# Kernel tuning notes

Hardware: AMD Instinct MI355X
Metric: run time of the kernel (lower is better)

## Reference

```python
import jax, jax.numpy as jnp
import numpy as np

N, IN_DIM, EMB = 65536, 768, 128
CB_SIZES = [8, 64, 512]
COMMIT = 0.25  # standard EMA-VQ commitment cost


def setup_inputs() -> dict:
    key = jax.random.key(0)
    ks = jax.random.split(key, 12)
    s = 0.02
    return {
        "x": jax.random.normal(ks[0], (N, IN_DIM), jnp.float32),
        "W_e1": jax.random.normal(ks[1], (IN_DIM, IN_DIM), jnp.float32) * s,
        "b_e1": jnp.zeros((IN_DIM,), jnp.float32),
        "W_e2": jax.random.normal(ks[2], (EMB, IN_DIM), jnp.float32) * s,
        "b_e2": jnp.zeros((EMB,), jnp.float32),
        "W_d1": jax.random.normal(ks[3], (EMB, EMB), jnp.float32) * s,
        "b_d1": jnp.zeros((EMB,), jnp.float32),
        "W_d2": jax.random.normal(ks[4], (EMB, EMB), jnp.float32) * s,
        "b_d2": jnp.zeros((EMB,), jnp.float32),
        "E0": jax.random.normal(ks[5], (CB_SIZES[0], EMB), jnp.float32),
        "E1": jax.random.normal(ks[6], (CB_SIZES[1], EMB), jnp.float32),
        "E2": jax.random.normal(ks[7], (CB_SIZES[2], EMB), jnp.float32),
    }


def _quantize(r, E):
    # squared L2 distances [N, K] = |r|^2 - 2 r.E^T + |E|^2
    d = (jnp.sum(r * r, axis=-1, keepdims=True)
         - 2.0 * jnp.einsum("nd,kd->nk", r, E)
         + jnp.sum(E * E, axis=-1))
    idx = jnp.argmin(d, axis=-1)          # [N]
    z_q = E[idx]                           # gather [N, EMB]
    loss = COMMIT * jnp.mean((jax.lax.stop_gradient(z_q) - r) ** 2)
    z_q_st = r + jax.lax.stop_gradient(z_q - r)  # straight-through
    return z_q_st, loss, idx


def reference(x, W_e1, b_e1, W_e2, b_e2, W_d1, b_d1, W_d2, b_d2, E0, E1, E2):
    # encoder MLP
    h = jax.nn.relu(x @ W_e1.T + b_e1)
    z = h @ W_e2.T + b_e2                 # [N, EMB]

    residual = z
    quantized_sum = jnp.zeros_like(z)
    total_loss = jnp.float32(0.0)
    all_indices = []
    for E in (E0, E1, E2):                # fixed depth=3 residual VQ loop
        z_q, loss, idx = _quantize(residual, E)
        residual = residual - z_q
        quantized_sum = quantized_sum + z_q
        total_loss = total_loss + loss
        all_indices.append(idx)

    # decoder MLP
    h2 = jax.nn.relu(quantized_sum @ W_d1.T + b_d1)
    reconstructed = h2 @ W_d2.T + b_d2    # [N, EMB]
    codes = jnp.stack(all_indices, axis=1)  # [N, depth]
    return reconstructed, total_loss, codes
```

## Files before the change

### kernel.cpp

```cpp
#include <hip/hip_runtime.h>

typedef _Float16 f16;
typedef __attribute__((ext_vector_type(4))) _Float16 f16x4;
typedef __attribute__((ext_vector_type(8))) _Float16 f16x8;
typedef __attribute__((ext_vector_type(4))) float    f32x4;

static constexpr int NROWS = 65536;
static constexpr int D_IN  = 768;
static constexpr int D_EMB = 128;
static constexpr long LOSS_OFF  = (long)NROWS * D_EMB;
static constexpr long CODES_OFF = LOSS_OFF + 1;

static constexpr long WOFF = 201326592L;
static constexpr long WE1H = 0,       WE1L = 589824;
static constexpr long WE2H = 1179648, WE2L = 1277952;
static constexpr long WD1F = 1376256, WD2F = 1392640;
static constexpr long E0H = 1409024, E0L = 1410048;
static constexpr long E1H = 1411072, E1L = 1419264;
static constexpr long E2H = 1427456, E2L = 1492992;
static constexpr long PARTIAL_B = WOFF + 4194304L;
static constexpr long NORM_B    = WOFF + 4198400L;

__device__ __forceinline__ float dot4(float4 a, float4 b){
  return fmaf(a.x,b.x, fmaf(a.y,b.y, fmaf(a.z,b.z, a.w*b.w)));
}

__device__ __forceinline__ void split4(float4 v, f16x4& hi, f16x4& lo){
  _Float16 h0=(_Float16)v.x, h1=(_Float16)v.y, h2=(_Float16)v.z, h3=(_Float16)v.w;
  hi[0]=h0; hi[1]=h1; hi[2]=h2; hi[3]=h3;
  lo[0]=(_Float16)((v.x-(float)h0)*2048.0f);
  lo[1]=(_Float16)((v.y-(float)h1)*2048.0f);
  lo[2]=(_Float16)((v.z-(float)h2)*2048.0f);
  lo[3]=(_Float16)((v.w-(float)h3)*2048.0f);
}

__device__ __forceinline__ void split8_reg(const float* v, f16x8& hi, f16x8& lo){
#pragma unroll
  for (int i = 0; i < 8; i++){
    _Float16 h = (_Float16)v[i];
    hi[i] = h;
    lo[i] = (_Float16)((v[i]-(float)h)*2048.0f);
  }
}

__global__ __launch_bounds__(256)
void split_weights_kernel(const float* __restrict__ We1, const float* __restrict__ We2,
                          const float* __restrict__ Wd1, const float* __restrict__ Wd2,
                          const float* __restrict__ E0,  const float* __restrict__ E1,
                          const float* __restrict__ E2,  f16* __restrict__ wp){
  int t = blockIdx.x*256 + threadIdx.x;
  if (t >= 198912) return;
  const float* src; long o4; long hO, lO; bool dual = true;
  if      (t < 147456){ src=We1; o4=t;        hO=WE1H; lO=WE1L; }
  else if (t < 172032){ src=We2; o4=t-147456; hO=WE2H; lO=WE2L; }
  else if (t < 176128){ src=Wd1; o4=t-172032; hO=WD1F; lO=0; dual=false; }
  else if (t < 180224){ src=Wd2; o4=t-176128; hO=WD2F; lO=0; dual=false; }
  else if (t < 180480){ src=E0;  o4=t-180224; hO=E0H;  lO=E0L; }
  else if (t < 182528){ src=E1;  o4=t-180480; hO=E1H;  lO=E1L; }
  else                { src=E2;  o4=t-182528; hO=E2H;  lO=E2L; }
  float4 v = *(const float4*)(src + o4*4);
  if (dual){
    f16x4 h4, l4; split4(v, h4, l4);
    *(f16x4*)(wp + hO + o4*4) = h4;
    *(f16x4*)(wp + lO + o4*4) = l4;
  } else {
    f16x4 h4; h4[0]=(_Float16)v.x; h4[1]=(_Float16)v.y; h4[2]=(_Float16)v.z; h4[3]=(_Float16)v.w;
    *(f16x4*)(wp + hO + o4*4) = h4;
  }
}

__global__ __launch_bounds__(256)
void enorm_kernel(const float* __restrict__ E0, const float* __restrict__ E1,
                  const float* __restrict__ E2, float* __restrict__ norms){
  int t = blockIdx.x*256 + threadIdx.x;
  if (t >= 584) return;
  const float* row;
  if (t < 8)       row = E0 + (long)t*128;
  else if (t < 72) row = E1 + (long)(t-8)*128;
  else             row = E2 + (long)(t-72)*128;
  float q[4];
#pragma unroll
  for (int sq = 0; sq < 4; sq++){
    float s = 0.f;
#pragma unroll
    for (int j = 0; j < 8; j++){
      float4 v = *(const float4*)(row + sq*32 + j*4);
      s += dot4(v, v);
    }
    q[sq] = s;
  }
  norms[t] = ((q[0] + q[1]) + q[2]) + q[3];
}

template<bool RELU>
__global__ __launch_bounds__(512, 2)
void gemm_v2_kernel(const float* __restrict__ A,
                    const f16* __restrict__ Bhg, const f16* __restrict__ Blg,
                    const float* __restrict__ bias, float* __restrict__ C,
                    int M, int N, int K){
  constexpr int RS = 40;
  __shared__ f16 AhL[2][256*RS];
  __shared__ f16 AlL[2][256*RS];
  __shared__ f16 BhL[2][128*RS];
  __shared__ f16 BlL[2][128*RS];

  const int tid = threadIdx.x;
  const int wave = tid >> 6, lane = tid & 63;
  const int wm = wave >> 1, wn = wave & 1;
  const int lr = lane & 15, lg = lane >> 4;

  const int gx  = gridDim.x;
  const int lid = blockIdx.y * gx + blockIdx.x;
  const int xcd = lid & 7;
  const int rr  = lid >> 3;
  const int bx  = rr % gx;
  const int by  = (rr / gx) * 8 + xcd;

  const long m0 = (long)by * 256;
  const long n0 = (long)bx * 128;

  const int ar = tid >> 3;
  const int ac = tid & 7;
  const int br = tid >> 2;
  const int bkc = tid & 3;

  const int nt = K >> 5;

  float4 pa[4];
  f16x8 pbh, pbl;

#pragma unroll
  for (int i = 0; i < 4; i++)
    pa[i] = *(const float4*)(A + (m0 + i*64 + ar)*K + ac*4);
  pbh = *(const f16x8*)(Bhg + (n0 + br)*K + bkc*8);
  pbl = *(const f16x8*)(Blg + (n0 + br)*K + bkc*8);

#pragma unroll
  for (int i = 0; i < 4; i++){
    f16x4 h4, l4; split4(pa[i], h4, l4);
    *(f16x4*)&AhL[0][(i*64 + ar)*RS + ac*4] = h4;
    *(f16x4*)&AlL[0][(i*64 + ar)*RS + ac*4] = l4;
  }
  *(f16x8*)&BhL[0][br*RS + bkc*8] = pbh;
  *(f16x8*)&BlL[0][br*RS + bkc*8] = pbl;
  __syncthreads();

  f32x4 accm[4][4], accc[4][4];
#pragma unroll
  for (int i = 0; i < 4; i++)
#pragma unroll
    for (int j = 0; j < 4; j++){
      accm[i][j] = (f32x4){0.f,0.f,0.f,0.f};
      accc[i][j] = (f32x4){0.f,0.f,0.f,0.f};
    }

  int cur = 0;
  for (int t = 0; t < nt; t++){
    const bool more = (t + 1 < nt);
    if (more){
      const long ko = (long)(t+1) * 32;
#pragma unroll
      for (int i = 0; i < 4; i++)
        pa[i] = *(const float4*)(A + (m0 + i*64 + ar)*K + ko + ac*4);
      pbh = *(const f16x8*)(Bhg + (n0 + br)*K + ko + bkc*8);
      pbl = *(const f16x8*)(Blg + (n0 + br)*K + ko + bkc*8);
    }

    f16x8 ah[4], al[4];
#pragma unroll
    for (int mi = 0; mi < 4; mi++){
      int row = wm*64 + mi*16 + lr;
      ah[mi] = *(const f16x8*)&AhL[cur][row*RS + lg*8];
      al[mi] = *(const f16x8*)&AlL[cur][row*RS + lg*8];
    }
#pragma unroll
    for (int ni = 0; ni < 4; ni++){
      int col = wn*64 + ni*16 + lr;
      f16x8 bh = *(const f16x8*)&BhL[cur][col*RS + lg*8];
      f16x8 bl = *(const f16x8*)&BlL[cur][col*RS + lg*8];
#pragma unroll
      for (int mi = 0; mi < 4; mi++){
        accm[mi][ni] = __builtin_amdgcn_mfma_f32_16x16x32_f16(ah[mi], bh, accm[mi][ni], 0, 0, 0);
        accc[mi][ni] = __builtin_amdgcn_mfma_f32_16x16x32_f16(ah[mi], bl, accc[mi][ni], 0, 0, 0);
        accc[mi][ni] = __builtin_amdgcn_mfma_f32_16x16x32_f16(al[mi], bh, accc[mi][ni], 0, 0, 0);
      }
    }

    if (more){
      int nb = cur ^ 1;
#pragma unroll
      for (int i = 0; i < 4; i++){
        f16x4 h4, l4; split4(pa[i], h4, l4);
        *(f16x4*)&AhL[nb][(i*64 + ar)*RS + ac*4] = h4;
        *(f16x4*)&AlL[nb][(i*64 + ar)*RS + ac*4] = l4;
      }
      *(f16x8*)&BhL[nb][br*RS + bkc*8] = pbh;
      *(f16x8*)&BlL[nb][br*RS + bkc*8] = pbl;
      __syncthreads();
      cur = nb;
    }
  }

  float bv[4];
#pragma unroll
  for (int ni = 0; ni < 4; ni++) bv[ni] = bias[n0 + wn*64 + ni*16 + lr];
#pragma unroll
  for (int mi = 0; mi < 4; mi++){
#pragma unroll
    for (int ni = 0; ni < 4; ni++){
#pragma unroll
      for (int r = 0; r < 4; r++){
        float v = accm[mi][ni][r] + accc[mi][ni][r]*(1.0f/2048.0f) + bv[ni];
        if (RELU) v = fmaxf(v, 0.f);
        long row = m0 + wm*64 + mi*16 + lg*4 + r;
        C[row*N + n0 + wn*64 + ni*16 + lr] = v;
      }
    }
  }
}

template<bool RELU, bool OUT16>
__global__ __launch_bounds__(256)
void gemm_f16_dec(const f16* __restrict__ Ag, const f16* __restrict__ Bg,
                  const float* __restrict__ bias,
                  float* __restrict__ C32, f16* __restrict__ C16, int M){
  constexpr int RS = 136;
  __shared__ f16 As[128*RS];
  __shared__ f16 Bs[128*RS];
  const int tid = threadIdx.x;
  const int wave = tid >> 6, lane = tid & 63;
  const int wm = wave >> 1, wn = wave & 1;
  const int lr = lane & 15, lg = lane >> 4;
  const long m0 = (long)blockIdx.y * 128;
  const int srow = tid >> 1, sco = (tid & 1) * 64;

#pragma unroll
  for (int c = 0; c < 8; c++){
    *(f16x8*)&As[srow*RS + sco + c*8] = *(const f16x8*)(Ag + (m0+srow)*128 + sco + c*8);
    *(f16x8*)&Bs[srow*RS + sco + c*8] = *(const f16x8*)(Bg + (long)srow*128 + sco + c*8);
  }
  __syncthreads();

  f32x4 acc[4][4];
#pragma unroll
  for (int i = 0; i < 4; i++)
#pragma unroll
    for (int j = 0; j < 4; j++) acc[i][j] = (f32x4){0.f,0.f,0.f,0.f};

#pragma unroll
  for (int ks = 0; ks < 4; ks++){
    f16x8 a[4];
#pragma unroll
    for (int mi = 0; mi < 4; mi++)
      a[mi] = *(const f16x8*)&As[(wm*64 + mi*16 + lr)*RS + ks*32 + lg*8];
#pragma unroll
    for (int ni = 0; ni < 4; ni++){
      f16x8 b = *(const f16x8*)&Bs[(wn*64 + ni*16 + lr)*RS + ks*32 + lg*8];
#pragma unroll
      for (int mi = 0; mi < 4; mi++)
        acc[mi][ni] = __builtin_amdgcn_mfma_f32_16x16x32_f16(a[mi], b, acc[mi][ni], 0, 0, 0);
    }
  }

  float bv[4];
#pragma unroll
  for (int ni = 0; ni < 4; ni++) bv[ni] = bias[wn*64 + ni*16 + lr];
#pragma unroll
  for (int mi = 0; mi < 4; mi++){
#pragma unroll
    for (int ni = 0; ni < 4; ni++){
#pragma unroll
      for (int r = 0; r < 4; r++){
        float v = acc[mi][ni][r] + bv[ni];
        if (RELU) v = fmaxf(v, 0.f);
        long row = m0 + wm*64 + mi*16 + lg*4 + r;
        long col = wn*64 + ni*16 + lr;
        if (OUT16) C16[row*128 + col] = (_Float16)v;
        else       C32[row*128 + col] = v;
      }
    }
  }
}

__global__ __launch_bounds__(256)
void vq_mfma_kernel(const float* __restrict__ z,
                    const float* __restrict__ E0c, const float* __restrict__ E1c,
                    const float* __restrict__ E2c,
                    const f16* __restrict__ wp, const float* __restrict__ normg,
                    f16* __restrict__ q16, float* __restrict__ out,
                    float* __restrict__ partial){
  constexpr int VS = 132;
  constexpr int ES = 136;
  __shared__ float rs[64*VS];
  __shared__ f16 Eh[64*ES];
  __shared__ f16 El[64*ES];
  __shared__ float pE[64];
  __shared__ int   besti[3*64];
  __shared__ float wsum[4];

  const int tid  = threadIdx.x;
  const int wave = tid >> 6, lane = tid & 63;
  const int lr = lane & 15, lg = lane >> 4;
  const int row0 = blockIdx.x * 64;
  const int urow = tid & 63, uq = tid >> 6;
  const int sc = tid & 63, sq = tid >> 6;

#pragma unroll
  for (int i = 0; i < 8; i++){
    int idx = i*256 + tid;
    int r = idx >> 5, c = (idx & 31) * 4;
    *(float4*)&rs[r*VS + c] = *(const float4*)&z[(long)(row0 + r)*D_EMB + c];
  }

  float4 qa[8];
#pragma unroll
  for (int j = 0; j < 8; j++) qa[j] = make_float4(0.f,0.f,0.f,0.f);
  float lsum = 0.f;

  const float* Etab[3] = {E0c, E1c, E2c};
  const int    Ktab[3] = {8, 64, 512};
  const long   EHt[3]  = {E0H, E1H, E2H};
  const long   ELt[3]  = {E0L, E1L, E2L};
  const int    NOt[3]  = {0, 8, 72};

  for (int l = 0; l < 3; l++){
    const float* E = Etab[l];
    const int K = Ktab[l];
    const f16* Ehg = wp + EHt[l];
    const f16* Elg = wp + ELt[l];
    const float* nrm = normg + NOt[l];

    __syncthreads();
    f16x8 ah[4], al[4];
#pragma unroll
    for (int ks = 0; ks < 4; ks++){
      float av[8];
      *(float4*)&av[0] = *(const float4*)&rs[(wave*16 + lr)*VS + ks*32 + lg*8];
      *(float4*)&av[4] = *(const float4*)&rs[(wave*16 + lr)*VS + ks*32 + lg*8 + 4];
      split8_reg(av, ah[ks], al[ks]);
    }

    float bd[4]; int bi[4];
#pragma unroll
    for (int r = 0; r < 4; r++){ bd[r] = 3.0e38f; bi[r] = 0x7fffffff; }

    for (int kbase = 0; kbase < K; kbase += 64){
      const int cn = (K - kbase < 64) ? (K - kbase) : 64;
      __syncthreads();
      if (sc < cn){
        long go = (long)(kbase + sc)*D_EMB + sq*32;
#pragma unroll
        for (int j = 0; j < 4; j++){
          *(f16x8*)&Eh[sc*ES + sq*32 + j*8] = *(const f16x8*)(Ehg + go + j*8);
          *(f16x8*)&El[sc*ES + sq*32 + j*8] = *(const f16x8*)(Elg + go + j*8);
        }
        if (sq == 0) pE[sc] = nrm[kbase + sc];
      } else {
        f16x8 zz;
#pragma unroll
        for (int i = 0; i < 8; i++) zz[i] = (_Float16)0.f;
#pragma unroll
        for (int j = 0; j < 4; j++){
          *(f16x8*)&Eh[sc*ES + sq*32 + j*8] = zz;
          *(f16x8*)&El[sc*ES + sq*32 + j*8] = zz;
        }
        if (sq == 0) pE[sc] = 3.0e38f;
      }
      __syncthreads();

      const int cgmax = (cn + 15) >> 4;
      for (int cg = 0; cg < cgmax; cg++){
        f32x4 Sm = (f32x4){0.f,0.f,0.f,0.f};
        f32x4 Sc = (f32x4){0.f,0.f,0.f,0.f};
#pragma unroll
        for (int ks = 0; ks < 4; ks++){
          f16x8 bh = *(const f16x8*)&Eh[(cg*16 + lr)*ES + ks*32 + lg*8];
          f16x8 bl = *(const f16x8*)&El[(cg*16 + lr)*ES + ks*32 + lg*8];
          Sm = __builtin_amdgcn_mfma_f32_16x16x32_f16(ah[ks], bh, Sm, 0, 0, 0);
          Sc = __builtin_amdgcn_mfma_f32_16x16x32_f16(ah[ks], bl, Sc, 0, 0, 0);
          Sc = __builtin_amdgcn_mfma_f32_16x16x32_f16(al[ks], bh, Sc, 0, 0, 0);
        }
        int code = cg*16 + lr;
        float ne = pE[code];
        int kg = kbase + code;
#pragma unroll
        for (int r = 0; r < 4; r++){
          float S  = fmaf(Sc[r], 1.0f/2048.0f, Sm[r]);
          float sd = fmaf(-2.0f, S, ne);
          if (sd < bd[r]){ bd[r] = sd; bi[r] = kg; }
        }
      }
    }

#pragma unroll
    for (int r = 0; r < 4; r++){
#pragma unroll
      for (int off = 1; off < 16; off <<= 1){
        float ob = __shfl_xor(bd[r], off, 16);
        int   oi = __shfl_xor(bi[r], off, 16);
        if (ob < bd[r] || (ob == bd[r] && oi < bi[r])){ bd[r] = ob; bi[r] = oi; }
      }
      if (lr == 0) besti[l*64 + wave*16 + lg*4 + r] = bi[r];
    }
    __syncthreads();

    {
      int k = besti[l*64 + urow];
      const float* Er = E + (long)k*D_EMB + uq*32;
#pragma unroll
      for (int j = 0; j < 8; j++){
        float4 e = *(const float4*)&Er[j*4];
        float* rp = &rs[urow*VS + uq*32 + j*4];
        float4 r = *(const float4*)rp;
        float4 df = make_float4(e.x-r.x, e.y-r.y, e.z-r.z, e.w-r.w);
        lsum += dot4(df, df);
        *(float4*)rp = make_float4(r.x-e.x, r.y-e.y, r.z-e.z, r.w-e.w);
        qa[j].x += e.x; qa[j].y += e.y; qa[j].z += e.z; qa[j].w += e.w;
      }
    }
  }

  __syncthreads();
#pragma unroll
  for (int j = 0; j < 8; j++)
    *(float4*)&rs[urow*VS + uq*32 + j*4] = qa[j];
  __syncthreads();
#pragma unroll
  for (int i = 0; i < 8; i++){
    int idx = i*256 + tid;
    int r = idx >> 5, c = (idx & 31) * 4;
    float4 v = *(const float4*)&rs[r*VS + c];
    f16x4 h4; h4[0]=(_Float16)v.x; h4[1]=(_Float16)v.y; h4[2]=(_Float16)v.z; h4[3]=(_Float16)v.w;
    *(f16x4*)&q16[(long)(row0 + r)*D_EMB + c] = h4;
  }
  if (tid < 64){
    long n = row0 + tid;
    for (int l = 0; l < 3; l++)
      out[CODES_OFF + n*3 + l] = (float)besti[l*64 + tid];
  }
  for (int off = 32; off > 0; off >>= 1) lsum += __shfl_down(lsum, off);
  if ((tid & 63) == 0) wsum[tid >> 6] = lsum;
  __syncthreads();
  if (tid == 0) partial[blockIdx.x] = wsum[0] + wsum[1] + wsum[2] + wsum[3];
}

__global__ __launch_bounds__(256)
void loss_reduce_kernel(const float* __restrict__ partial, float* __restrict__ out){
  __shared__ float ws2[4];
  int tid = threadIdx.x;
  float s = 0.f;
  for (int i = tid; i < 1024; i += 256) s += partial[i];
  for (int off = 32; off > 0; off >>= 1) s += __shfl_down(s, off);
  if ((tid & 63) == 0) ws2[tid >> 6] = s;
  __syncthreads();
  if (tid == 0)
    out[LOSS_OFF] = (ws2[0] + ws2[1] + ws2[2] + ws2[3]) * (0.25f / (float)((long)NROWS * D_EMB));
}

extern "C" void kernel_launch(void* const* d_in, const int* in_sizes, int n_in,
                              void* d_out, int out_size, void* d_ws, size_t ws_size,
                              hipStream_t stream) {
  (void)in_sizes; (void)n_in; (void)out_size; (void)ws_size;
  const float* x   = (const float*)d_in[0];
  const float* We1 = (const float*)d_in[1];
  const float* be1 = (const float*)d_in[2];
  const float* We2 = (const float*)d_in[3];
  const float* be2 = (const float*)d_in[4];
  const float* Wd1 = (const float*)d_in[5];
  const float* bd1 = (const float*)d_in[6];
  const float* Wd2 = (const float*)d_in[7];
  const float* bd2 = (const float*)d_in[8];
  const float* E0  = (const float*)d_in[9];
  const float* E1  = (const float*)d_in[10];
  const float* E2  = (const float*)d_in[11];
  float* out = (float*)d_out;
  char*  ws  = (char*)d_ws;

  float* h    = (float*)ws;
  f16*   q16  = (f16*)ws;
  f16*   h216 = (f16*)(ws + 33554432L);
  f16*   wp   = (f16*)(ws + WOFF);
  float* partial = (float*)(ws + PARTIAL_B);
  float* norms   = (float*)(ws + NORM_B);
  float* z = out;

  dim3 blk(256);
  split_weights_kernel<<<dim3(777), blk, 0, stream>>>(We1, We2, Wd1, Wd2, E0, E1, E2, wp);
  enorm_kernel<<<dim3(3), blk, 0, stream>>>(E0, E1, E2, norms);
  gemm_v2_kernel<true ><<<dim3(D_IN/128,  NROWS/256), dim3(512), 0, stream>>>(
      x, wp+WE1H, wp+WE1L, be1, h, NROWS, D_IN,  D_IN);
  gemm_v2_kernel<false><<<dim3(D_EMB/128, NROWS/256), dim3(512), 0, stream>>>(
      h, wp+WE2H, wp+WE2L, be2, z, NROWS, D_EMB, D_IN);
  vq_mfma_kernel<<<dim3(NROWS/64), blk, 0, stream>>>(z, E0, E1, E2, wp, norms, q16, out, partial);
  loss_reduce_kernel<<<dim3(1), blk, 0, stream>>>(partial, out);
  gemm_f16_dec<true, true ><<<dim3(1, NROWS/128), blk, 0, stream>>>(q16,  wp+WD1F, bd1, nullptr, h216, NROWS);
  gemm_f16_dec<false,false><<<dim3(1, NROWS/128), blk, 0, stream>>>(h216, wp+WD2F, bd2, out, nullptr, NROWS);
}
```

Before: 454.1 us.

## Fuse encoder second GEMM, residual VQ and decoder MLP into one kernel

Replaces the separate z-GEMM, VQ and two decoder GEMM launches with one kernel per 128-row tile. The kernel computes z with a split-fp16 MFMA GEMM over h, runs the three-level quantization on the LDS-resident residual, then applies both decoder layers from shared memory. This removes the global round trips of z, q16 and h2 and three kernel launches. The cost is a large LDS arena (about 134 KB), which limits occupancy to one block per CU. The z GEMM now runs on only 512 blocks, each covering all 128 output columns.

```diff
diff --git a/kernel.cpp b/kernel.cpp
--- a/kernel.cpp
+++ b/kernel.cpp
@@ -219,103 +219,152 @@
   }
 }
 
-template<bool RELU, bool OUT16>
 __global__ __launch_bounds__(256)
-void gemm_f16_dec(const f16* __restrict__ Ag, const f16* __restrict__ Bg,
-                  const float* __restrict__ bias,
-                  float* __restrict__ C32, f16* __restrict__ C16, int M){
-  constexpr int RS = 136;
-  __shared__ f16 As[128*RS];
-  __shared__ f16 Bs[128*RS];
-  const int tid = threadIdx.x;
+void fused_zvqdec_kernel(const float* __restrict__ hg,
+                         const f16* __restrict__ Bhg, const f16* __restrict__ Blg,
+                         const float* __restrict__ be2,
+                         const float* __restrict__ E0c, const float* __restrict__ E1c,
+                         const float* __restrict__ E2c,
+                         const f16* __restrict__ wp, const float* __restrict__ normg,
+                         const float* __restrict__ bd1g, const float* __restrict__ bd2g,
+                         float* __restrict__ out, float* __restrict__ partial){
+  __shared__ __align__(16) char arena[137280];
+  constexpr int VS = 132;
+  constexpr int ES = 136;
+
+  const int tid  = threadIdx.x;
   const int wave = tid >> 6, lane = tid & 63;
   const int wm = wave >> 1, wn = wave & 1;
   const int lr = lane & 15, lg = lane >> 4;
-  const long m0 = (long)blockIdx.y * 128;
-  const int srow = tid >> 1, sco = (tid & 1) * 64;
-
-#pragma unroll
-  for (int c = 0; c < 8; c++){
-    *(f16x8*)&As[srow*RS + sco + c*8] = *(const f16x8*)(Ag + (m0+srow)*128 + sco + c*8);
-    *(f16x8*)&Bs[srow*RS + sco + c*8] = *(const f16x8*)(Bg + (long)srow*128 + sco + c*8);
-  }
-  __syncthreads();
-
-  f32x4 acc[4][4];
-#pragma unroll
-  for (int i = 0; i < 4; i++)
-#pragma unroll
-    for (int j = 0; j < 4; j++) acc[i][j] = (f32x4){0.f,0.f,0.f,0.f};
-
-#pragma unroll
-  for (int ks = 0; ks < 4; ks++){
-    f16x8 a[4];
+  const long row0 = (long)blockIdx.x * 128;
+
+  float* rs = (float*)arena;
+  f16*  Eh  = (f16*)(arena + 67584);
+  f16*  El  = (f16*)(arena + 84992);
+  float* pE = (float*)(arena + 102400);
+  int*  besti = (int*)(arena + 102656);
+  float* wsum = (float*)(arena + 104192);
+  f16*  W1  = (f16*)(arena + 67584);
+  f16*  W2  = (f16*)(arena + 102400);
+  f16*  h2p = (f16*)arena;
+
+  {
+    constexpr int RS = 40;
+    f16* base = (f16*)arena;
+    f16* AhL = base;
+    f16* AlL = base + 10240;
+    f16* BhL = base + 20480;
+    f16* BlL = base + 30720;
+    const int K = D_IN;
+    const int srow = tid >> 3, sc4 = tid & 7;
+    const int prow = tid >> 1, pkc = (tid & 1)*2;
+
+    float4 pa[4];
+    f16x8 pbh[2], pbl[2];
+#pragma unroll
+    for (int p = 0; p < 4; p++)
+      pa[p] = *(const float4*)(hg + (row0 + p*32 + srow)*K + sc4*4);
+#pragma unroll
+    for (int c = 0; c < 2; c++){
+      pbh[c] = *(const f16x8*)(Bhg + (long)prow*K + (pkc+c)*8);
+      pbl[c] = *(const f16x8*)(Blg + (long)prow*K + (pkc+c)*8);
+    }
+#pragma unroll
+    for (int p = 0; p < 4; p++){
+      f16x4 h4, l4; split4(pa[p], h4, l4);
+      *(f16x4*)&AhL[(p*32 + srow)*RS + sc4*4] = h4;
+      *(f16x4*)&AlL[(p*32 + srow)*RS + sc4*4] = l4;
+    }
+#pragma unroll
+    for (int c = 0; c < 2; c++){
+      *(f16x8*)&BhL[prow*RS + (pkc+c)*8] = pbh[c];
+      *(f16x8*)&BlL[prow*RS + (pkc+c)*8] = pbl[c];
+    }
+    __syncthreads();
+
+    f32x4 accm[4][4], accc[4][4];
+#pragma unroll
+    for (int i = 0; i < 4; i++)
+#pragma unroll
+      for (int j = 0; j < 4; j++){
+        accm[i][j] = (f32x4){0.f,0.f,0.f,0.f};
+        accc[i][j] = (f32x4){0.f,0.f,0.f,0.f};
+      }
+
+    const int nt = K >> 5;
+    int cur = 0;
+    for (int t = 0; t < nt; t++){
+      const bool more = (t + 1 < nt);
+      if (more){
+        const long ko = (long)(t+1)*32;
+#pragma unroll
+        for (int p = 0; p < 4; p++)
+          pa[p] = *(const float4*)(hg + (row0 + p*32 + srow)*K + ko + sc4*4);
+#pragma unroll
+        for (int c = 0; c < 2; c++){
+          pbh[c] = *(const f16x8*)(Bhg + (long)prow*K + ko + (pkc+c)*8);
+          pbl[c] = *(const f16x8*)(Blg + (long)prow*K + ko + (pkc+c)*8);
+        }
+      }
+      f16x8 ah[4], al[4];
+#pragma unroll
+      for (int mi = 0; mi < 4; mi++){
+        int row = wm*64 + mi*16 + lr;
+        ah[mi] = *(const f16x8*)&AhL[cur*5120 + row*RS + lg*8];
+        al[mi] = *(const f16x8*)&AlL[cur*5120 + row*RS + lg*8];
+      }
+#pragma unroll
+      for (int ni = 0; ni < 4; ni++){
+        int col = wn*64 + ni*16 + lr;
+        f16x8 bh = *(const f16x8*)&BhL[cur*5120 + col*RS + lg*8];
+        f16x8 bl = *(const f16x8*)&BlL[cur*5120 + col*RS + lg*8];
+#pragma unroll
+        for (int mi = 0; mi < 4; mi++){
+          accm[mi][ni] = __builtin_amdgcn_mfma_f32_16x16x32_f16(ah[mi], bh, accm[mi][ni], 0, 0, 0);
+          accc[mi][ni] = __builtin_amdgcn_mfma_f32_16x16x32_f16(ah[mi], bl, accc[mi][ni], 0, 0, 0);
+          accc[mi][ni] = __builtin_amdgcn_mfma_f32_16x16x32_f16(al[mi], bh, accc[mi][ni], 0, 0, 0);
+        }
+      }
+      if (more){
+        int nb = cur ^ 1;
+#pragma unroll
+        for (int p = 0; p < 4; p++){
+          f16x4 h4, l4; split4(pa[p], h4, l4);
+          *(f16x4*)&AhL[nb*5120 + (p*32 + srow)*RS + sc4*4] = h4;
+          *(f16x4*)&AlL[nb*5120 + (p*32 + srow)*RS + sc4*4] = l4;
+        }
+#pragma unroll
+        for (int c = 0; c < 2; c++){
+          *(f16x8*)&BhL[nb*5120 + prow*RS + (pkc+c)*8] = pbh[c];
+          *(f16x8*)&BlL[nb*5120 + prow*RS + (pkc+c)*8] = pbl[c];
+        }
+        __syncthreads();
+        cur = nb;
+      }
+    }
+
+    __syncthreads();
+    float bv[4];
+#pragma unroll
+    for (int ni = 0; ni < 4; ni++) bv[ni] = be2[wn*64 + ni*16 + lr];
 #pragma unroll
     for (int mi = 0; mi < 4; mi++)
-      a[mi] = *(const f16x8*)&As[(wm*64 + mi*16 + lr)*RS + ks*32 + lg*8];
-#pragma unroll
-    for (int ni = 0; ni < 4; ni++){
-      f16x8 b = *(const f16x8*)&Bs[(wn*64 + ni*16 + lr)*RS + ks*32 + lg*8];
-#pragma unroll
-      for (int mi = 0; mi < 4; mi++)
-        acc[mi][ni] = __builtin_amdgcn_mfma_f32_16x16x32_f16(a[mi], b, acc[mi][ni], 0, 0, 0);
-    }
-  }
-
-  float bv[4];
-#pragma unroll
-  for (int ni = 0; ni < 4; ni++) bv[ni] = bias[wn*64 + ni*16 + lr];
-#pragma unroll
-  for (int mi = 0; mi < 4; mi++){
-#pragma unroll
-    for (int ni = 0; ni < 4; ni++){
-#pragma unroll
-      for (int r = 0; r < 4; r++){
-        float v = acc[mi][ni][r] + bv[ni];
-        if (RELU) v = fmaxf(v, 0.f);
-        long row = m0 + wm*64 + mi*16 + lg*4 + r;
-        long col = wn*64 + ni*16 + lr;
-        if (OUT16) C16[row*128 + col] = (_Float16)v;
-        else       C32[row*128 + col] = v;
-      }
-    }
-  }
-}
-
-__global__ __launch_bounds__(256)
-void vq_mfma_kernel(const float* __restrict__ z,
-                    const float* __restrict__ E0c, const float* __restrict__ E1c,
-                    const float* __restrict__ E2c,
-                    const f16* __restrict__ wp, const float* __restrict__ normg,
-                    f16* __restrict__ q16, float* __restrict__ out,
-                    float* __restrict__ partial){
-  constexpr int VS = 132;
-  constexpr int ES = 136;
-  __shared__ float rs[64*VS];
-  __shared__ f16 Eh[64*ES];
-  __shared__ f16 El[64*ES];
-  __shared__ float pE[64];
-  __shared__ int   besti[3*64];
-  __shared__ float wsum[4];
-
-  const int tid  = threadIdx.x;
-  const int wave = tid >> 6, lane = tid & 63;
-  const int lr = lane & 15, lg = lane >> 4;
-  const int row0 = blockIdx.x * 64;
-  const int urow = tid & 63, uq = tid >> 6;
+#pragma unroll
+      for (int ni = 0; ni < 4; ni++)
+#pragma unroll
+        for (int r = 0; r < 4; r++){
+          float v = accm[mi][ni][r] + accc[mi][ni][r]*(1.0f/2048.0f) + bv[ni];
+          rs[(wm*64 + mi*16 + lg*4 + r)*VS + wn*64 + ni*16 + lr] = v;
+        }
+  }
+
+  float4 qa[16];
+#pragma unroll
+  for (int j = 0; j < 16; j++) qa[j] = make_float4(0.f,0.f,0.f,0.f);
+  float lsum = 0.f;
+
+  const int urow = tid & 127, uh = tid >> 7;
   const int sc = tid & 63, sq = tid >> 6;
-
-#pragma unroll
-  for (int i = 0; i < 8; i++){
-    int idx = i*256 + tid;
-    int r = idx >> 5, c = (idx & 31) * 4;
-    *(float4*)&rs[r*VS + c] = *(const float4*)&z[(long)(row0 + r)*D_EMB + c];
-  }
-
-  float4 qa[8];
-#pragma unroll
-  for (int j = 0; j < 8; j++) qa[j] = make_float4(0.f,0.f,0.f,0.f);
-  float lsum = 0.f;
 
   const float* Etab[3] = {E0c, E1c, E2c};
   const int    Ktab[3] = {8, 64, 512};
@@ -331,18 +380,22 @@
     const float* nrm = normg + NOt[l];
 
     __syncthreads();
-    f16x8 ah[4], al[4];
-#pragma unroll
-    for (int ks = 0; ks < 4; ks++){
-      float av[8];
-      *(float4*)&av[0] = *(const float4*)&rs[(wave*16 + lr)*VS + ks*32 + lg*8];
-      *(float4*)&av[4] = *(const float4*)&rs[(wave*16 + lr)*VS + ks*32 + lg*8 + 4];
-      split8_reg(av, ah[ks], al[ks]);
-    }
-
-    float bd[4]; int bi[4];
-#pragma unroll
-    for (int r = 0; r < 4; r++){ bd[r] = 3.0e38f; bi[r] = 0x7fffffff; }
+    f16x8 ah[2][4], al[2][4];
+#pragma unroll
+    for (int rg = 0; rg < 2; rg++)
+#pragma unroll
+      for (int ks = 0; ks < 4; ks++){
+        float av[8];
+        *(float4*)&av[0] = *(const float4*)&rs[(wave*32 + rg*16 + lr)*VS + ks*32 + lg*8];
+        *(float4*)&av[4] = *(const float4*)&rs[(wave*32 + rg*16 + lr)*VS + ks*32 + lg*8 + 4];
+        split8_reg(av, ah[rg][ks], al[rg][ks]);
+      }
+
+    float bd[2][4]; int bi[2][4];
+#pragma unroll
+    for (int rg = 0; rg < 2; rg++)
+#pragma unroll
+      for (int r = 0; r < 4; r++){ bd[rg][r] = 3.0e38f; bi[rg][r] = 0x7fffffff; }
 
     for (int kbase = 0; kbase < K; kbase += 64){
       const int cn = (K - kbase < 64) ? (K - kbase) : 64;
@@ -370,47 +423,58 @@
 
       const int cgmax = (cn + 15) >> 4;
       for (int cg = 0; cg < cgmax; cg++){
-        f32x4 Sm = (f32x4){0.f,0.f,0.f,0.f};
-        f32x4 Sc = (f32x4){0.f,0.f,0.f,0.f};
+        f32x4 Sm[2], Sc2[2];
+#pragma unroll
+        for (int rg = 0; rg < 2; rg++){
+          Sm[rg]  = (f32x4){0.f,0.f,0.f,0.f};
+          Sc2[rg] = (f32x4){0.f,0.f,0.f,0.f};
+        }
 #pragma unroll
         for (int ks = 0; ks < 4; ks++){
           f16x8 bh = *(const f16x8*)&Eh[(cg*16 + lr)*ES + ks*32 + lg*8];
           f16x8 bl = *(const f16x8*)&El[(cg*16 + lr)*ES + ks*32 + lg*8];
-          Sm = __builtin_amdgcn_mfma_f32_16x16x32_f16(ah[ks], bh, Sm, 0, 0, 0);
-          Sc = __builtin_amdgcn_mfma_f32_16x16x32_f16(ah[ks], bl, Sc, 0, 0, 0);
-          Sc = __builtin_amdgcn_mfma_f32_16x16x32_f16(al[ks], bh, Sc, 0, 0, 0);
+#pragma unroll
+          for (int rg = 0; rg < 2; rg++){
+            Sm[rg]  = __builtin_amdgcn_mfma_f32_16x16x32_f16(ah[rg][ks], bh, Sm[rg], 0, 0, 0);
+            Sc2[rg] = __builtin_amdgcn_mfma_f32_16x16x32_f16(ah[rg][ks], bl, Sc2[rg], 0, 0, 0);
+            Sc2[rg] = __builtin_amdgcn_mfma_f32_16x16x32_f16(al[rg][ks], bh, Sc2[rg], 0, 0, 0);
+          }
         }
         int code = cg*16 + lr;
         float ne = pE[code];
         int kg = kbase + code;
 #pragma unroll
-        for (int r = 0; r < 4; r++){
-          float S  = fmaf(Sc[r], 1.0f/2048.0f, Sm[r]);
-          float sd = fmaf(-2.0f, S, ne);
-          if (sd < bd[r]){ bd[r] = sd; bi[r] = kg; }
-        }
-      }
-    }
-
-#pragma unroll
-    for (int r = 0; r < 4; r++){
-#pragma unroll
-      for (int off = 1; off < 16; off <<= 1){
-        float ob = __shfl_xor(bd[r], off, 16);
-        int   oi = __shfl_xor(bi[r], off, 16);
-        if (ob < bd[r] || (ob == bd[r] && oi < bi[r])){ bd[r] = ob; bi[r] = oi; }
-      }
-      if (lr == 0) besti[l*64 + wave*16 + lg*4 + r] = bi[r];
-    }
+        for (int rg = 0; rg < 2; rg++)
+#pragma unroll
+          for (int r = 0; r < 4; r++){
+            float S  = fmaf(Sc2[rg][r], 1.0f/2048.0f, Sm[rg][r]);
+            float sd = fmaf(-2.0f, S, ne);
+            if (sd < bd[rg][r]){ bd[rg][r] = sd; bi[rg][r] = kg; }
+          }
+      }
+    }
+
+#pragma unroll
+    for (int rg = 0; rg < 2; rg++)
+#pragma unroll
+      for (int r = 0; r < 4; r++){
+#pragma unroll
+        for (int off = 1; off < 16; off <<= 1){
+          float ob = __shfl_xor(bd[rg][r], off, 16);
+          int   oi = __shfl_xor(bi[rg][r], off, 16);
+          if (ob < bd[rg][r] || (ob == bd[rg][r] && oi < bi[rg][r])){ bd[rg][r] = ob; bi[rg][r] = oi; }
+        }
+        if (lr == 0) besti[l*128 + wave*32 + rg*16 + lg*4 + r] = bi[rg][r];
+      }
     __syncthreads();
 
     {
-      int k = besti[l*64 + urow];
-      const float* Er = E + (long)k*D_EMB + uq*32;
-#pragma unroll
-      for (int j = 0; j < 8; j++){
+      int k = besti[l*128 + urow];
+      const float* Er = E + (long)k*D_EMB + uh*64;
+#pragma unroll
+      for (int j = 0; j < 16; j++){
         float4 e = *(const float4*)&Er[j*4];
-        float* rp = &rs[urow*VS + uq*32 + j*4];
+        float* rp = &rs[urow*VS + uh*64 + j*4];
         float4 r = *(const float4*)rp;
         float4 df = make_float4(e.x-r.x, e.y-r.y, e.z-r.z, e.w-r.w);
         lsum += dot4(df, df);
@@ -420,28 +484,100 @@
     }
   }
 
-  __syncthreads();
-#pragma unroll
-  for (int j = 0; j < 8; j++)
-    *(float4*)&rs[urow*VS + uq*32 + j*4] = qa[j];
-  __syncthreads();
-#pragma unroll
-  for (int i = 0; i < 8; i++){
-    int idx = i*256 + tid;
-    int r = idx >> 5, c = (idx & 31) * 4;
-    float4 v = *(const float4*)&rs[r*VS + c];
-    f16x4 h4; h4[0]=(_Float16)v.x; h4[1]=(_Float16)v.y; h4[2]=(_Float16)v.z; h4[3]=(_Float16)v.w;
-    *(f16x4*)&q16[(long)(row0 + r)*D_EMB + c] = h4;
-  }
-  if (tid < 64){
+  if (tid < 128){
     long n = row0 + tid;
     for (int l = 0; l < 3; l++)
-      out[CODES_OFF + n*3 + l] = (float)besti[l*64 + tid];
+      out[CODES_OFF + n*3 + l] = (float)besti[l*128 + tid];
   }
   for (int off = 32; off > 0; off >>= 1) lsum += __shfl_down(lsum, off);
-  if ((tid & 63) == 0) wsum[tid >> 6] = lsum;
+  if ((tid & 63) == 0) wsum[wave] = lsum;
   __syncthreads();
   if (tid == 0) partial[blockIdx.x] = wsum[0] + wsum[1] + wsum[2] + wsum[3];
+#pragma unroll
+  for (int j = 0; j < 16; j++)
+    *(float4*)&rs[urow*VS + uh*64 + j*4] = qa[j];
+  __syncthreads();
+
+  {
+    const int srow = tid >> 1, sco = (tid & 1)*64;
+#pragma unroll
+    for (int c = 0; c < 8; c++){
+      *(f16x8*)&W1[srow*ES + sco + c*8] = *(const f16x8*)(wp + WD1F + (long)srow*128 + sco + c*8);
+      *(f16x8*)&W2[srow*ES + sco + c*8] = *(const f16x8*)(wp + WD2F + (long)srow*128 + sco + c*8);
+    }
+    f16x8 a1[2][4];
+#pragma unroll
+    for (int rg = 0; rg < 2; rg++)
+#pragma unroll
+      for (int ks = 0; ks < 4; ks++){
+        float av[8];
+        *(float4*)&av[0] = *(const float4*)&rs[(wave*32 + rg*16 + lr)*VS + ks*32 + lg*8];
+        *(float4*)&av[4] = *(const float4*)&rs[(wave*32 + rg*16 + lr)*VS + ks*32 + lg*8 + 4];
+#pragma unroll
+        for (int i = 0; i < 8; i++) a1[rg][ks][i] = (_Float16)av[i];
+      }
+    __syncthreads();
+
+    f32x4 acc[2][8];
+#pragma unroll
+    for (int rg = 0; rg < 2; rg++)
+#pragma unroll
+      for (int nf = 0; nf < 8; nf++) acc[rg][nf] = (f32x4){0.f,0.f,0.f,0.f};
+#pragma unroll
+    for (int ks = 0; ks < 4; ks++)
+#pragma unroll
+      for (int nf = 0; nf < 8; nf++){
+        f16x8 b = *(const f16x8*)&W1[(nf*16 + lr)*ES + ks*32 + lg*8];
+#pragma unroll
+        for (int rg = 0; rg < 2; rg++)
+          acc[rg][nf] = __builtin_amdgcn_mfma_f32_16x16x32_f16(a1[rg][ks], b, acc[rg][nf], 0, 0, 0);
+      }
+    float bv1[8];
+#pragma unroll
+    for (int nf = 0; nf < 8; nf++) bv1[nf] = bd1g[nf*16 + lr];
+#pragma unroll
+    for (int rg = 0; rg < 2; rg++)
+#pragma unroll
+      for (int nf = 0; nf < 8; nf++)
+#pragma unroll
+        for (int r = 0; r < 4; r++){
+          float v = fmaxf(acc[rg][nf][r] + bv1[nf], 0.f);
+          h2p[(wave*32 + rg*16 + lg*4 + r)*ES + nf*16 + lr] = (_Float16)v;
+        }
+    __syncthreads();
+
+    f16x8 a2[2][4];
+#pragma unroll
+    for (int rg = 0; rg < 2; rg++)
+#pragma unroll
+      for (int ks = 0; ks < 4; ks++)
+        a2[rg][ks] = *(const f16x8*)&h2p[(wave*32 + rg*16 + lr)*ES + ks*32 + lg*8];
+#pragma unroll
+    for (int rg = 0; rg < 2; rg++)
+#pragma unroll
+      for (int nf = 0; nf < 8; nf++) acc[rg][nf] = (f32x4){0.f,0.f,0.f,0.f};
+#pragma unroll
+    for (int ks = 0; ks < 4; ks++)
+#pragma unroll
+      for (int nf = 0; nf < 8; nf++){
+        f16x8 b = *(const f16x8*)&W2[(nf*16 + lr)*ES + ks*32 + lg*8];
+#pragma unroll
+        for (int rg = 0; rg < 2; rg++)
+          acc[rg][nf] = __builtin_amdgcn_mfma_f32_16x16x32_f16(a2[rg][ks], b, acc[rg][nf], 0, 0, 0);
+      }
+    float bv2[8];
+#pragma unroll
+    for (int nf = 0; nf < 8; nf++) bv2[nf] = bd2g[nf*16 + lr];
+#pragma unroll
+    for (int rg = 0; rg < 2; rg++)
+#pragma unroll
+      for (int nf = 0; nf < 8; nf++)
+#pragma unroll
+        for (int r = 0; r < 4; r++){
+          long row = row0 + wave*32 + rg*16 + lg*4 + r;
+          out[row*D_EMB + nf*16 + lr] = acc[rg][nf][r] + bv2[nf];
+        }
+  }
 }
 
 __global__ __launch_bounds__(256)
@@ -449,7 +585,7 @@
   __shared__ float ws2[4];
   int tid = threadIdx.x;
   float s = 0.f;
-  for (int i = tid; i < 1024; i += 256) s += partial[i];
+  for (int i = tid; i < 512; i += 256) s += partial[i];
   for (int off = 32; off > 0; off >>= 1) s += __shfl_down(s, off);
   if ((tid & 63) == 0) ws2[tid >> 6] = s;
   __syncthreads();
@@ -477,22 +613,16 @@
   char*  ws  = (char*)d_ws;
 
   float* h    = (float*)ws;
-  f16*   q16  = (f16*)ws;
-  f16*   h216 = (f16*)(ws + 33554432L);
   f16*   wp   = (f16*)(ws + WOFF);
   float* partial = (float*)(ws + PARTIAL_B);
   float* norms   = (float*)(ws + NORM_B);
-  float* z = out;
 
   dim3 blk(256);
   split_weights_kernel<<<dim3(777), blk, 0, stream>>>(We1, We2, Wd1, Wd2, E0, E1, E2, wp);
   enorm_kernel<<<dim3(3), blk, 0, stream>>>(E0, E1, E2, norms);
-  gemm_v2_kernel<true ><<<dim3(D_IN/128,  NROWS/256), dim3(512), 0, stream>>>(
-      x, wp+WE1H, wp+WE1L, be1, h, NROWS, D_IN,  D_IN);
-  gemm_v2_kernel<false><<<dim3(D_EMB/128, NROWS/256), dim3(512), 0, stream>>>(
-      h, wp+WE2H, wp+WE2L, be2, z, NROWS, D_EMB, D_IN);
-  vq_mfma_kernel<<<dim3(NROWS/64), blk, 0, stream>>>(z, E0, E1, E2, wp, norms, q16, out, partial);
+  gemm_v2_kernel<true><<<dim3(D_IN/128, NROWS/256), dim3(512), 0, stream>>>(
+      x, wp+WE1H, wp+WE1L, be1, h, NROWS, D_IN, D_IN);
+  fused_zvqdec_kernel<<<dim3(NROWS/128), blk, 0, stream>>>(
+      h, wp+WE2H, wp+WE2L, be2, E0, E1, E2, wp, norms, bd1, bd2, out, partial);
   loss_reduce_kernel<<<dim3(1), blk, 0, stream>>>(partial, out);
-  gemm_f16_dec<true, true ><<<dim3(1, NROWS/128), blk, 0, stream>>>(q16,  wp+WD1F, bd1, nullptr, h216, NROWS);
-  gemm_f16_dec<false,false><<<dim3(1, NROWS/128), blk, 0, stream>>>(h216, wp+WD2F, bd2, out, nullptr, NROWS);
-}
+}
```

Result: slower. 474.7 us (+4.5%).
